# Optimization experiments

Measured on AMD Instinct MI355X. Metric: run time of the kernel, lower is better.

The kernel has to match this reference:

```python
import jax, jax.numpy as jnp
import numpy as np

N = 10000
E = 320000
IN_CH = 256
OUT4 = 256  # 4 * out_channels, out_channels = 64


def setup_inputs() -> dict:
    key = jax.random.key(0)
    k1, k2, k3 = jax.random.split(key, 3)
    x = jax.random.normal(k1, (N, IN_CH), dtype=jnp.float32)
    edge_index = jax.random.randint(k2, (2, E), 0, N, dtype=jnp.int64)
    stdv = 1.0 / np.sqrt(64.0)  # 1/sqrt(out_channels), as in __init__
    weight = jax.random.uniform(k3, (IN_CH, OUT4), dtype=jnp.float32,
                                minval=-stdv, maxval=stdv)
    return {"x": x, "weight": weight, "edge_index": edge_index}


def reference(x, weight, edge_index):
    n = x.shape[0]
    idx = jnp.arange(n)
    # dense adjacency with self-loops (duplicates/edges just set to 1)
    adj = jnp.zeros((n, n), dtype=x.dtype)
    adj = adj.at[idx, idx].set(1.0)
    adj = adj.at[edge_index[0], edge_index[1]].set(1.0)
    # symmetric degree normalization D^-1/2 A D^-1/2
    deg = jnp.sum(adj, axis=1)  # >= 1 due to self-loops
    d_inv_sqrt = jax.lax.rsqrt(deg)
    norm_adj = adj * d_inv_sqrt[:, None] * d_inv_sqrt[None, :]
    # aggregate then project: (A_norm @ x) @ W
    return jnp.matmul(jnp.matmul(norm_adj, x), weight)
```

## Files before the change

kernel.cpp:

```cpp
#include <hip/hip_runtime.h>


#define CH 256
#define ELLW 96

typedef __attribute__((ext_vector_type(8))) short short8;
typedef __attribute__((ext_vector_type(4))) float f32x4;

__device__ inline unsigned short f2b(float f) {
    unsigned x = __builtin_bit_cast(unsigned, f);
    x = (x + 0x7fffu + ((x >> 16) & 1u)) >> 16;
    return (unsigned short)x;
}
__device__ inline float b2f(unsigned short u) {
    unsigned v = ((unsigned)u) << 16;
    return __builtin_bit_cast(float, v);
}

__global__ void clear_cnt_kernel(int* cnt, int n) {
    int i = blockIdx.x * blockDim.x + threadIdx.x;
    if (i < n) cnt[i] = 0;
}

__global__ void fill_kernel(const int* __restrict__ ei, int e_cnt,
                            int* cnt, int* __restrict__ col_ell,
                            const float* __restrict__ w,
                            unsigned short* __restrict__ wt) {
    int t = blockIdx.x * blockDim.x + threadIdx.x;
    if (t < e_cnt) {
        int r = ei[t];
        int c = ei[e_cnt + t];
        int pos = atomicAdd(&cnt[r], 1);
        if (pos < ELLW) col_ell[(size_t)r * ELLW + pos] = c;
    } else if (t < e_cnt + CH * CH) {
        int idx = t - e_cnt;
        int k = idx >> 8, nn = idx & 255;
        wt[nn * CH + k] = f2b(w[idx]);
    }
}

__global__ __launch_bounds__(256) void dedup_kernel(
    int* cnt, int* __restrict__ col_ell, int* __restrict__ deg, int n) {
    __shared__ int sh[4][ELLW];
    const int wv = threadIdx.x >> 6, lane = threadIdx.x & 63;
    const int r = blockIdx.x * 4 + wv;

    int m = 0;
    if (r < n) { m = cnt[r]; if (m > ELLW) m = ELLW; }
    for (int e = lane; e < m; e += 64) sh[wv][e] = col_ell[(size_t)r * ELLW + e];
    __syncthreads();

    if (r < n) {
        const int e0 = lane, e1 = 64 + lane;
        int c0 = (e0 < m) ? sh[wv][e0] : -1;
        int c1 = (e1 < m) ? sh[wv][e1] : -1;
        bool dup0 = (c0 == r), dup1 = (c1 == r);
        for (int k = 0; k < m; ++k) {
            int ck = sh[wv][k];
            dup0 |= (k < e0) && (ck == c0);
            dup1 |= (k < e1) && (ck == c1);
        }
        unsigned long long b0 = __ballot((e0 < m) && !dup0);
        unsigned long long b1 = __ballot((e1 < m) && !dup1);
        unsigned long long lt = (1ull << lane) - 1ull;
        int n0 = __popcll(b0);
        int mm = n0 + __popcll(b1);
        if (mm != m) {
            if ((e0 < m) && !dup0)
                col_ell[(size_t)r * ELLW + __popcll(b0 & lt)] = c0;
            if ((e1 < m) && !dup1)
                col_ell[(size_t)r * ELLW + n0 + __popcll(b1 & lt)] = c1;
            if (lane == 0) cnt[r] = mm;
        }
        if (lane == 0) deg[r] = mm + 1;
    }
}

__global__ __launch_bounds__(256) void gemm_kernel(
    const float* __restrict__ x, const unsigned short* __restrict__ wt,
    const int* __restrict__ deg, unsigned short* __restrict__ zb, int n) {
    const int tid = threadIdx.x;
    const int lane = tid & 63;
    const int wv = tid >> 6;
    const int m0 = blockIdx.x * 16;
    const int n0 = wv * 64;
    const int rsel = lane & 15;
    const int kbase = (lane >> 4) * 8;

    const float* xrow = x + (size_t)(m0 + rsel) * CH + kbase;
    const unsigned short* b0p = wt + (size_t)(n0 + rsel) * CH + kbase;
    const unsigned short* b1p = b0p + 16 * CH;
    const unsigned short* b2p = b0p + 32 * CH;
    const unsigned short* b3p = b0p + 48 * CH;

    f32x4 acc0 = {0.f, 0.f, 0.f, 0.f};
    f32x4 acc1 = acc0, acc2 = acc0, acc3 = acc0;

#pragma unroll
    for (int kc = 0; kc < 8; ++kc) {
        const float4* p = (const float4*)(xrow + kc * 32);
        float4 u = p[0], v = p[1];
        short8 a;
        a[0] = (short)f2b(u.x); a[1] = (short)f2b(u.y);
        a[2] = (short)f2b(u.z); a[3] = (short)f2b(u.w);
        a[4] = (short)f2b(v.x); a[5] = (short)f2b(v.y);
        a[6] = (short)f2b(v.z); a[7] = (short)f2b(v.w);
        short8 b0 = *(const short8*)(b0p + kc * 32);
        short8 b1 = *(const short8*)(b1p + kc * 32);
        short8 b2 = *(const short8*)(b2p + kc * 32);
        short8 b3 = *(const short8*)(b3p + kc * 32);
        acc0 = __builtin_amdgcn_mfma_f32_16x16x32_bf16(a, b0, acc0, 0, 0, 0);
        acc1 = __builtin_amdgcn_mfma_f32_16x16x32_bf16(a, b1, acc1, 0, 0, 0);
        acc2 = __builtin_amdgcn_mfma_f32_16x16x32_bf16(a, b2, acc2, 0, 0, 0);
        acc3 = __builtin_amdgcn_mfma_f32_16x16x32_bf16(a, b3, acc3, 0, 0, 0);
    }

    const int r0 = (lane >> 4) * 4;
    int4 dg = *(const int4*)(deg + m0 + r0);
    float dvj[4] = {rsqrtf((float)dg.x), rsqrtf((float)dg.y),
                    rsqrtf((float)dg.z), rsqrtf((float)dg.w)};
#pragma unroll
    for (int j = 0; j < 4; ++j) {
        unsigned short* zr = zb + (size_t)(m0 + r0 + j) * CH + n0 + rsel;
        zr[0]  = f2b(acc0[j] * dvj[j]);
        zr[16] = f2b(acc1[j] * dvj[j]);
        zr[32] = f2b(acc2[j] * dvj[j]);
        zr[48] = f2b(acc3[j] * dvj[j]);
    }
}

__global__ __launch_bounds__(256) void gather_kernel(
    const int* __restrict__ cnt, const int* __restrict__ col_ell,
    const int* __restrict__ deg,
    const unsigned short* __restrict__ zb, float* __restrict__ out, int n) {
    int wid = (blockIdx.x * blockDim.x + threadIdx.x) >> 6;
    if (wid >= n) return;
    const int lane = threadIdx.x & 63;
    const int half = lane >> 5;
    const int chb = (lane & 31) * 8;
    const int m = cnt[wid];
    const int* cl = col_ell + (size_t)wid * ELLW;

    float acc[8];
    if (half == 0) {
        short8 s = *(const short8*)(zb + (size_t)wid * CH + chb);
#pragma unroll
        for (int i = 0; i < 8; ++i) acc[i] = b2f((unsigned short)s[i]);
    } else {
#pragma unroll
        for (int i = 0; i < 8; ++i) acc[i] = 0.f;
    }

    int idx = half;
    for (; idx + 6 < m; idx += 8) {
        int c0 = cl[idx], c1 = cl[idx + 2], c2 = cl[idx + 4], c3 = cl[idx + 6];
        short8 v0 = *(const short8*)(zb + (size_t)c0 * CH + chb);
        short8 v1 = *(const short8*)(zb + (size_t)c1 * CH + chb);
        short8 v2 = *(const short8*)(zb + (size_t)c2 * CH + chb);
        short8 v3 = *(const short8*)(zb + (size_t)c3 * CH + chb);
#pragma unroll
        for (int i = 0; i < 8; ++i)
            acc[i] += b2f((unsigned short)v0[i]) + b2f((unsigned short)v1[i])
                    + b2f((unsigned short)v2[i]) + b2f((unsigned short)v3[i]);
    }
    for (; idx < m; idx += 2) {
        int c = cl[idx];
        short8 v = *(const short8*)(zb + (size_t)c * CH + chb);
#pragma unroll
        for (int i = 0; i < 8; ++i) acc[i] += b2f((unsigned short)v[i]);
    }

#pragma unroll
    for (int i = 0; i < 8; ++i) acc[i] += __shfl_xor(acc[i], 32);

    float d = rsqrtf((float)deg[wid]);
    float4 o;
    if (half == 0) { o.x = acc[0]; o.y = acc[1]; o.z = acc[2]; o.w = acc[3]; }
    else           { o.x = acc[4]; o.y = acc[5]; o.z = acc[6]; o.w = acc[7]; }
    o.x *= d; o.y *= d; o.z *= d; o.w *= d;
    *(float4*)(out + (size_t)wid * CH + chb + half * 4) = o;
}

extern "C" void kernel_launch(void* const* d_in, const int* in_sizes, int n_in,
                              void* d_out, int out_size, void* d_ws, size_t ws_size,
                              hipStream_t stream) {
    const float* x = (const float*)d_in[0];
    const float* w = (const float*)d_in[1];
    const int* ei = (const int*)d_in[2];
    float* out = (float*)d_out;

    const int n = in_sizes[0] / CH;
    const int e_cnt = in_sizes[2] / 2;

    char* ws = (char*)d_ws;
    size_t off = 0;
    unsigned short* zb = (unsigned short*)(ws + off); off += (size_t)n * CH * 2;
    unsigned short* wt = (unsigned short*)(ws + off); off += (size_t)CH * CH * 2;
    int* cnt = (int*)(ws + off);     off += (size_t)n * 4;
    int* deg = (int*)(ws + off);     off += (size_t)n * 4;
    int* col_ell = (int*)(ws + off); off += (size_t)n * ELLW * 4;

    clear_cnt_kernel<<<(n + 255) / 256, 256, 0, stream>>>(cnt, n);

    int total = e_cnt + CH * CH;
    fill_kernel<<<(total + 255) / 256, 256, 0, stream>>>(ei, e_cnt, cnt, col_ell, w, wt);
    dedup_kernel<<<(n + 3) / 4, 256, 0, stream>>>(cnt, col_ell, deg, n);
    gemm_kernel<<<n / 16, 256, 0, stream>>>(x, wt, deg, zb, n);
    gather_kernel<<<(n * 64 + 255) / 256, 256, 0, stream>>>(cnt, col_ell, deg, zb, out, n);
}
```

Measured before the change: 80.59 us.

## Split intermediate into two channel slices and gather per slice with 4-way edge split

The GEMM now writes the bf16 projected features in two 128-channel slabs (slice-major) instead of one 256-wide row. The gather launches two wavefronts per node, one per slab, with each wave splitting edges four ways and reducing through two shuffle stages. The aim is a smaller per-pass working set in cache (5 MB per slab) and more parallelism for the latency-bound random gathers. In exchange, neighbor index lists are read twice and there is extra shuffle reduction; the neighbor count is also clamped to the ELL width.

```diff
diff --git a/kernel.cpp b/kernel.cpp
--- a/kernel.cpp
+++ b/kernel.cpp
@@ -119,9 +119,11 @@
     int4 dg = *(const int4*)(deg + m0 + r0);
     float dvj[4] = {rsqrtf((float)dg.x), rsqrtf((float)dg.y),
                     rsqrtf((float)dg.z), rsqrtf((float)dg.w)};
+    const int slice = n0 >> 7;
+    const int nn0 = n0 & 127;
 #pragma unroll
     for (int j = 0; j < 4; ++j) {
-        unsigned short* zr = zb + (size_t)(m0 + r0 + j) * CH + n0 + rsel;
+        unsigned short* zr = zb + ((size_t)slice * n + (m0 + r0 + j)) * 128 + nn0 + rsel;
         zr[0]  = f2b(acc0[j] * dvj[j]);
         zr[16] = f2b(acc1[j] * dvj[j]);
         zr[32] = f2b(acc2[j] * dvj[j]);
@@ -133,17 +135,20 @@
     const int* __restrict__ cnt, const int* __restrict__ col_ell,
     const int* __restrict__ deg,
     const unsigned short* __restrict__ zb, float* __restrict__ out, int n) {
-    int wid = (blockIdx.x * blockDim.x + threadIdx.x) >> 6;
-    if (wid >= n) return;
+    int wgid = (blockIdx.x * blockDim.x + threadIdx.x) >> 6;
+    if (wgid >= 2 * n) return;
+    const int slice = (wgid >= n) ? 1 : 0;
+    const int wid = wgid - slice * n;
     const int lane = threadIdx.x & 63;
-    const int half = lane >> 5;
-    const int chb = (lane & 31) * 8;
-    const int m = cnt[wid];
+    const int g = lane >> 4;
+    const int chb = (lane & 15) * 8;
+    int m = cnt[wid]; if (m > ELLW) m = ELLW;
     const int* cl = col_ell + (size_t)wid * ELLW;
+    const unsigned short* zs = zb + (size_t)slice * n * 128 + chb;
 
     float acc[8];
-    if (half == 0) {
-        short8 s = *(const short8*)(zb + (size_t)wid * CH + chb);
+    if (g == 0) {
+        short8 s = *(const short8*)(zs + (size_t)wid * 128);
 #pragma unroll
         for (int i = 0; i < 8; ++i) acc[i] = b2f((unsigned short)s[i]);
     } else {
@@ -151,34 +156,39 @@
         for (int i = 0; i < 8; ++i) acc[i] = 0.f;
     }
 
-    int idx = half;
-    for (; idx + 6 < m; idx += 8) {
-        int c0 = cl[idx], c1 = cl[idx + 2], c2 = cl[idx + 4], c3 = cl[idx + 6];
-        short8 v0 = *(const short8*)(zb + (size_t)c0 * CH + chb);
-        short8 v1 = *(const short8*)(zb + (size_t)c1 * CH + chb);
-        short8 v2 = *(const short8*)(zb + (size_t)c2 * CH + chb);
-        short8 v3 = *(const short8*)(zb + (size_t)c3 * CH + chb);
-#pragma unroll
-        for (int i = 0; i < 8; ++i)
-            acc[i] += b2f((unsigned short)v0[i]) + b2f((unsigned short)v1[i])
-                    + b2f((unsigned short)v2[i]) + b2f((unsigned short)v3[i]);
-    }
-    for (; idx < m; idx += 2) {
+    int idx = g;
+    for (; idx + 12 < m; idx += 16) {
+        int c0 = cl[idx], c1 = cl[idx + 4], c2 = cl[idx + 8], c3 = cl[idx + 12];
+        short8 v0 = *(const short8*)(zs + (size_t)c0 * 128);
+        short8 v1 = *(const short8*)(zs + (size_t)c1 * 128);
+        short8 v2 = *(const short8*)(zs + (size_t)c2 * 128);
+        short8 v3 = *(const short8*)(zs + (size_t)c3 * 128);
+#pragma unroll
+        for (int q = 0; q < 8; ++q)
+            acc[q] += b2f((unsigned short)v0[q]) + b2f((unsigned short)v1[q])
+                    + b2f((unsigned short)v2[q]) + b2f((unsigned short)v3[q]);
+    }
+    for (; idx < m; idx += 4) {
         int c = cl[idx];
-        short8 v = *(const short8*)(zb + (size_t)c * CH + chb);
-#pragma unroll
-        for (int i = 0; i < 8; ++i) acc[i] += b2f((unsigned short)v[i]);
-    }
-
+        short8 v = *(const short8*)(zs + (size_t)c * 128);
+#pragma unroll
+        for (int q = 0; q < 8; ++q) acc[q] += b2f((unsigned short)v[q]);
+    }
+
+#pragma unroll
+    for (int i = 0; i < 8; ++i) acc[i] += __shfl_xor(acc[i], 16);
 #pragma unroll
     for (int i = 0; i < 8; ++i) acc[i] += __shfl_xor(acc[i], 32);
 
-    float d = rsqrtf((float)deg[wid]);
-    float4 o;
-    if (half == 0) { o.x = acc[0]; o.y = acc[1]; o.z = acc[2]; o.w = acc[3]; }
-    else           { o.x = acc[4]; o.y = acc[5]; o.z = acc[6]; o.w = acc[7]; }
-    o.x *= d; o.y *= d; o.z *= d; o.w *= d;
-    *(float4*)(out + (size_t)wid * CH + chb + half * 4) = o;
+    if (g == 0) {
+        float d = rsqrtf((float)deg[wid]);
+        float* dst = out + (size_t)wid * CH + slice * 128 + chb;
+        float4 o0, o1;
+        o0.x = acc[0] * d; o0.y = acc[1] * d; o0.z = acc[2] * d; o0.w = acc[3] * d;
+        o1.x = acc[4] * d; o1.y = acc[5] * d; o1.z = acc[6] * d; o1.w = acc[7] * d;
+        *(float4*)dst = o0;
+        *(float4*)(dst + 4) = o1;
+    }
 }
 
 extern "C" void kernel_launch(void* const* d_in, const int* in_sizes, int n_in,
@@ -206,5 +216,5 @@
     fill_kernel<<<(total + 255) / 256, 256, 0, stream>>>(ei, e_cnt, cnt, col_ell, w, wt);
     dedup_kernel<<<(n + 3) / 4, 256, 0, stream>>>(cnt, col_ell, deg, n);
     gemm_kernel<<<n / 16, 256, 0, stream>>>(x, wt, deg, zb, n);
-    gather_kernel<<<(n * 64 + 255) / 256, 256, 0, stream>>>(cnt, col_ell, deg, zb, out, n);
-}
+    gather_kernel<<<(2 * n * 64 + 255) / 256, 256, 0, stream>>>(cnt, col_ell, deg, zb, out, n);
+}
```

Result: no change. 80.45 us (-0.2%).
